# Kernel optimization log

Hardware: AMD Instinct MI355X
Metric: run time of the kernel (lower is better)

Reference implementation:

```python
import jax, jax.numpy as jnp
import numpy as np

NUM_HEADS = 4
SCALE = 0.1767766952966369  # head_dim**-0.5, head_dim=32


def setup_inputs() -> dict:
    key = jax.random.key(0)
    k1, k2, k3 = jax.random.split(key, 3)
    B, N, C = 4096, 49, 384  # B = 64 images * 64 windows, N = 7*7, C = 3*embed_dims
    qkv = jax.random.normal(k1, (B, N, C), dtype=jnp.float32)
    mask = jax.random.normal(k2, (NUM_HEADS, N, N), dtype=jnp.float32)
    rotate_mask = jax.random.normal(k3, (64, N, N), dtype=jnp.float32)  # nW = 64
    hw_pad = jnp.array([56, 56], dtype=jnp.int32)  # metadata only, unused in math
    return {"qkv": qkv, "mask": mask, "rotate_mask": rotate_mask, "hw_pad": hw_pad}


def reference(qkv, mask, rotate_mask, hw_pad):
    B, N, C = qkv.shape
    H = NUM_HEADS
    hd = C // H // 3
    # [B,N,3,H,hd] -> [3,B,H,N,hd]
    qkv_r = qkv.reshape(B, N, 3, H, hd).transpose(2, 0, 3, 1, 4)
    q, k, v = qkv_r[0] * SCALE, qkv_r[1], qkv_r[2]
    attn = jnp.einsum('bhqd,bhkd->bhqk', q, k) + mask  # mask broadcasts over B
    nW = rotate_mask.shape[0]
    # shifted-window mask: add per-window rotate mask, broadcast over image batch and heads
    attn = attn.reshape(B // nW, nW, H, N, N) + rotate_mask[None, :, None, :, :]
    attn = jax.nn.softmax(attn.reshape(B, H, N, N), axis=-1)
    out = jnp.einsum('bhqk,bhkd->bhqd', attn, v)  # [B,H,N,hd]
    return out.transpose(0, 2, 1, 3).reshape(B, N, C // 3)
```

## Files before the change

kernel.cpp:

```cpp
#include <hip/hip_runtime.h>

#define NTOK 49
#define NH 4
#define HD 32
#define CIN 384
#define NW 64
#define NPAD 64
#define QKP 136
#define SCALE_F 0.1767766952966369f

typedef _Float16 f16x8 __attribute__((ext_vector_type(8)));
typedef float f32x16 __attribute__((ext_vector_type(16)));
typedef __fp16 fp16x2 __attribute__((ext_vector_type(2)));

__device__ __forceinline__ unsigned int pkh(float a, float b) {
    fp16x2 h = __builtin_amdgcn_cvt_pkrtz(a, b);
    return __builtin_bit_cast(unsigned int, h);
}

__global__ __launch_bounds__(64) void prep_cmask(
    const float* __restrict__ mask,
    const float* __restrict__ rot,
    float* __restrict__ cmT)
{
    const int wh = blockIdx.x;
    const int w = wh >> 2, h = wh & 3;
    const int i = threadIdx.x;
    for (int j = 0; j < NPAD; ++j) {
        float v;
        if (j >= NTOK) v = -1e30f;
        else if (i >= NTOK) v = 0.f;
        else v = mask[(h * NTOK + i) * NTOK + j] + rot[(w * NTOK + i) * NTOK + j];
        cmT[((size_t)wh * NPAD + j) * NPAD + i] = v;
    }
}

template<bool USE_CM>
__global__ __launch_bounds__(512) void win_attn_mfma(
    const float* __restrict__ qkv,
    const float* __restrict__ mask,
    const float* __restrict__ rot,
    const float* __restrict__ cmT,
    float* __restrict__ out)
{
    const int b = blockIdx.x;
    const int w = b & (NW - 1);
    const int tid = threadIdx.x;
    const int wid = tid >> 6;
    const int h = wid >> 1;
    const int it = wid & 1;
    const int lane = tid & 63;
    const int l31 = lane & 31;
    const int hl = lane >> 5;

    __shared__ _Float16 Qs[NPAD * QKP];
    __shared__ _Float16 Ks[NPAD * QKP];

    const float* base = qkv + (size_t)b * (NTOK * CIN);

    for (int e = tid; e < NTOK * 64; e += 512) {
        const int n = e >> 6;
        const int c = e & 63;
        const int col = c * 4;
        const float4 f = *reinterpret_cast<const float4*>(base + n * CIN + col);
        uint2 u;
        if (col < 128) {
            u.x = pkh(f.x * SCALE_F, f.y * SCALE_F);
            u.y = pkh(f.z * SCALE_F, f.w * SCALE_F);
            *reinterpret_cast<uint2*>(&Qs[n * QKP + col]) = u;
        } else {
            u.x = pkh(f.x, f.y);
            u.y = pkh(f.z, f.w);
            *reinterpret_cast<uint2*>(&Ks[n * QKP + (col - 128)]) = u;
        }
    }
    for (int e = tid; e < 15 * 64; e += 512) {
        const int n = NTOK + (e >> 6);
        const int c = e & 63;
        const int col = c * 4;
        const uint2 z = make_uint2(0u, 0u);
        if (col < 128) *reinterpret_cast<uint2*>(&Qs[n * QKP + col]) = z;
        else           *reinterpret_cast<uint2*>(&Ks[n * QKP + (col - 128)]) = z;
    }

    const int i = l31 + 32 * it;
    float cm[2][16];
    #pragma unroll
    for (int jt = 0; jt < 2; ++jt) {
        #pragma unroll
        for (int r = 0; r < 16; ++r) {
            const int j = (r & 3) + 8 * (r >> 2) + 4 * hl + 32 * jt;
            if (USE_CM) {
                cm[jt][r] = cmT[((size_t)(w * 4 + h) * NPAD + j) * NPAD + i];
            } else {
                float v;
                if (j >= NTOK) v = -1e30f;
                else if (i >= NTOK) v = 0.f;
                else v = mask[(h * NTOK + i) * NTOK + j] + rot[(w * NTOK + i) * NTOK + j];
                cm[jt][r] = v;
            }
        }
    }

    __syncthreads();

    f16x8 ka[2][2], qa[2];
    #pragma unroll
    for (int kt = 0; kt < 2; ++kt) {
        #pragma unroll
        for (int ks = 0; ks < 2; ++ks) {
            ka[kt][ks] = *reinterpret_cast<const f16x8*>(&Ks[(l31 + 32 * kt) * QKP + h * HD + ks * 16 + hl * 8]);
        }
    }
    #pragma unroll
    for (int ks = 0; ks < 2; ++ks) {
        qa[ks] = *reinterpret_cast<const f16x8*>(&Qs[(l31 + 32 * it) * QKP + h * HD + ks * 16 + hl * 8]);
    }

    f32x16 acc[2];
    #pragma unroll
    for (int jt = 0; jt < 2; ++jt) {
        f32x16 a;
        #pragma unroll
        for (int r = 0; r < 16; ++r) a[r] = 0.f;
        a = __builtin_amdgcn_mfma_f32_32x32x16_f16(ka[jt][0], qa[0], a, 0, 0, 0);
        a = __builtin_amdgcn_mfma_f32_32x32x16_f16(ka[jt][1], qa[1], a, 0, 0, 0);
        acc[jt] = a;
    }

    float m = -3e38f;
    #pragma unroll
    for (int jt = 0; jt < 2; ++jt) {
        #pragma unroll
        for (int r = 0; r < 16; ++r) {
            acc[jt][r] += cm[jt][r];
            m = fmaxf(m, acc[jt][r]);
        }
    }
    m = fmaxf(m, __shfl_xor(m, 32));
    float s = 0.f;
    #pragma unroll
    for (int jt = 0; jt < 2; ++jt) {
        #pragma unroll
        for (int r = 0; r < 16; ++r) {
            const float e = __expf(acc[jt][r] - m);
            acc[jt][r] = e;
            s += e;
        }
    }
    s += __shfl_xor(s, 32);
    const float inv = 1.f / s;
    #pragma unroll
    for (int jt = 0; jt < 2; ++jt) {
        #pragma unroll
        for (int r = 0; r < 16; ++r) acc[jt][r] *= inv;
    }

    f32x16 oacc;
    #pragma unroll
    for (int r = 0; r < 16; ++r) oacc[r] = 0.f;

    #pragma unroll
    for (int ks = 0; ks < 4; ++ks) {
        unsigned int vd[4];
        #pragma unroll
        for (int ep = 0; ep < 4; ++ep) {
            const int j0 = 16 * ks + 8 * hl + 2 * ep;
            float v0 = 0.f, v1 = 0.f;
            if (j0 < NTOK)
                v0 = qkv[((size_t)b * NTOK + j0) * CIN + 256 + h * HD + l31];
            if (j0 + 1 < NTOK)
                v1 = qkv[((size_t)b * NTOK + j0 + 1) * CIN + 256 + h * HD + l31];
            vd[ep] = pkh(v0, v1);
        }
        uint4 vu = make_uint4(vd[0], vd[1], vd[2], vd[3]);
        const f16x8 vb = __builtin_bit_cast(f16x8, vu);

        const int jt = ks >> 1;
        const int r8 = 8 * (ks & 1);
        const unsigned lo0 = pkh(acc[jt][r8 + 0], acc[jt][r8 + 1]);
        const unsigned lo1 = pkh(acc[jt][r8 + 2], acc[jt][r8 + 3]);
        const unsigned hi0 = pkh(acc[jt][r8 + 4], acc[jt][r8 + 5]);
        const unsigned hi1 = pkh(acc[jt][r8 + 6], acc[jt][r8 + 7]);
        const unsigned x0 = hl ? lo0 : hi0;
        const unsigned x1 = hl ? lo1 : hi1;
        const unsigned y0 = (unsigned)__shfl_xor((int)x0, 32);
        const unsigned y1 = (unsigned)__shfl_xor((int)x1, 32);
        uint4 pu;
        pu.x = hl ? y0 : lo0;
        pu.y = hl ? y1 : lo1;
        pu.z = hl ? hi0 : y0;
        pu.w = hl ? hi1 : y1;
        const f16x8 pa = __builtin_bit_cast(f16x8, pu);
        oacc = __builtin_amdgcn_mfma_f32_32x32x16_f16(pa, vb, oacc, 0, 0, 0);
    }

    float* obase = out + (size_t)b * NTOK * (NH * HD) + h * HD + l31;
    #pragma unroll
    for (int r = 0; r < 16; ++r) {
        const int io = (r & 3) + 8 * (r >> 2) + 4 * hl + 32 * it;
        if (io < NTOK) obase[(size_t)io * (NH * HD)] = oacc[r];
    }
}

extern "C" void kernel_launch(void* const* d_in, const int* in_sizes, int n_in,
                              void* d_out, int out_size, void* d_ws, size_t ws_size,
                              hipStream_t stream) {
    const float* qkv  = (const float*)d_in[0];
    const float* mask = (const float*)d_in[1];
    const float* rot  = (const float*)d_in[2];
    float* out = (float*)d_out;

    const int Btot = in_sizes[0] / (NTOK * CIN);
    dim3 grid(Btot);

    const size_t cm_bytes = (size_t)NW * NH * NPAD * NPAD * sizeof(float);
    if (ws_size >= cm_bytes && d_ws != nullptr) {
        float* cmT = (float*)d_ws;
        prep_cmask<<<dim3(NW * NH), 64, 0, stream>>>(mask, rot, cmT);
        win_attn_mfma<true><<<grid, 512, 0, stream>>>(qkv, mask, rot, cmT, out);
    } else {
        win_attn_mfma<false><<<grid, 512, 0, stream>>>(qkv, mask, rot, nullptr, out);
    }
}
```

Baseline: 108.2 us.

## Stage V in shared memory with coalesced loads and fold mask into MFMA init

V is now loaded together with Q and K in one unrolled, coalesced float4 pass and converted to fp16 in shared memory. The old per-element strided global V reads inside the PV loop are removed. Zero-padding of rows 49-63 is merged into the same loop. The combined mask is used as the initial MFMA accumulator instead of being added afterward, which costs extra LDS and may lower occupancy.

```diff
diff --git a/kernel.cpp b/kernel.cpp
--- a/kernel.cpp
+++ b/kernel.cpp
@@ -6,7 +6,8 @@
 #define CIN 384
 #define NW 64
 #define NPAD 64
-#define QKP 136
+#define QS 136
+#define VS 132
 #define SCALE_F 0.1767766952966369f
 
 typedef _Float16 f16x8 __attribute__((ext_vector_type(8)));
@@ -53,34 +54,34 @@
     const int l31 = lane & 31;
     const int hl = lane >> 5;
 
-    __shared__ _Float16 Qs[NPAD * QKP];
-    __shared__ _Float16 Ks[NPAD * QKP];
+    __shared__ _Float16 Qs[NPAD * QS];
+    __shared__ _Float16 Ks[NPAD * QS];
+    __shared__ unsigned short Vs[NPAD * VS];
 
     const float* base = qkv + (size_t)b * (NTOK * CIN);
 
-    for (int e = tid; e < NTOK * 64; e += 512) {
-        const int n = e >> 6;
-        const int c = e & 63;
+    #pragma unroll
+    for (int t = 0; t < 12; ++t) {
+        const int e = tid + t * 512;
+        const int n = e / 96;
+        const int c = e % 96;
         const int col = c * 4;
-        const float4 f = *reinterpret_cast<const float4*>(base + n * CIN + col);
+        float4 f = make_float4(0.f, 0.f, 0.f, 0.f);
+        if (n < NTOK) f = *reinterpret_cast<const float4*>(base + n * CIN + col);
         uint2 u;
         if (col < 128) {
             u.x = pkh(f.x * SCALE_F, f.y * SCALE_F);
             u.y = pkh(f.z * SCALE_F, f.w * SCALE_F);
-            *reinterpret_cast<uint2*>(&Qs[n * QKP + col]) = u;
+            *reinterpret_cast<uint2*>(&Qs[n * QS + col]) = u;
+        } else if (col < 256) {
+            u.x = pkh(f.x, f.y);
+            u.y = pkh(f.z, f.w);
+            *reinterpret_cast<uint2*>(&Ks[n * QS + (col - 128)]) = u;
         } else {
             u.x = pkh(f.x, f.y);
             u.y = pkh(f.z, f.w);
-            *reinterpret_cast<uint2*>(&Ks[n * QKP + (col - 128)]) = u;
-        }
-    }
-    for (int e = tid; e < 15 * 64; e += 512) {
-        const int n = NTOK + (e >> 6);
-        const int c = e & 63;
-        const int col = c * 4;
-        const uint2 z = make_uint2(0u, 0u);
-        if (col < 128) *reinterpret_cast<uint2*>(&Qs[n * QKP + col]) = z;
-        else           *reinterpret_cast<uint2*>(&Ks[n * QKP + (col - 128)]) = z;
+            *reinterpret_cast<uint2*>(&Vs[n * VS + (col - 256)]) = u;
+        }
     }
 
     const int i = l31 + 32 * it;
@@ -109,12 +110,12 @@
     for (int kt = 0; kt < 2; ++kt) {
         #pragma unroll
         for (int ks = 0; ks < 2; ++ks) {
-            ka[kt][ks] = *reinterpret_cast<const f16x8*>(&Ks[(l31 + 32 * kt) * QKP + h * HD + ks * 16 + hl * 8]);
+            ka[kt][ks] = *reinterpret_cast<const f16x8*>(&Ks[(l31 + 32 * kt) * QS + h * HD + ks * 16 + hl * 8]);
         }
     }
     #pragma unroll
     for (int ks = 0; ks < 2; ++ks) {
-        qa[ks] = *reinterpret_cast<const f16x8*>(&Qs[(l31 + 32 * it) * QKP + h * HD + ks * 16 + hl * 8]);
+        qa[ks] = *reinterpret_cast<const f16x8*>(&Qs[(l31 + 32 * it) * QS + h * HD + ks * 16 + hl * 8]);
     }
 
     f32x16 acc[2];
@@ -122,7 +123,7 @@
     for (int jt = 0; jt < 2; ++jt) {
         f32x16 a;
         #pragma unroll
-        for (int r = 0; r < 16; ++r) a[r] = 0.f;
+        for (int r = 0; r < 16; ++r) a[r] = cm[jt][r];
         a = __builtin_amdgcn_mfma_f32_32x32x16_f16(ka[jt][0], qa[0], a, 0, 0, 0);
         a = __builtin_amdgcn_mfma_f32_32x32x16_f16(ka[jt][1], qa[1], a, 0, 0, 0);
         acc[jt] = a;
@@ -132,10 +133,7 @@
     #pragma unroll
     for (int jt = 0; jt < 2; ++jt) {
         #pragma unroll
-        for (int r = 0; r < 16; ++r) {
-            acc[jt][r] += cm[jt][r];
-            m = fmaxf(m, acc[jt][r]);
-        }
+        for (int r = 0; r < 16; ++r) m = fmaxf(m, acc[jt][r]);
     }
     m = fmaxf(m, __shfl_xor(m, 32));
     float s = 0.f;
@@ -164,14 +162,11 @@
     for (int ks = 0; ks < 4; ++ks) {
         unsigned int vd[4];
         #pragma unroll
-        for (int ep = 0; ep < 4; ++ep) {
-            const int j0 = 16 * ks + 8 * hl + 2 * ep;
-            float v0 = 0.f, v1 = 0.f;
-            if (j0 < NTOK)
-                v0 = qkv[((size_t)b * NTOK + j0) * CIN + 256 + h * HD + l31];
-            if (j0 + 1 < NTOK)
-                v1 = qkv[((size_t)b * NTOK + j0 + 1) * CIN + 256 + h * HD + l31];
-            vd[ep] = pkh(v0, v1);
+        for (int p = 0; p < 4; ++p) {
+            const int j0 = 16 * ks + 8 * hl + 2 * p;
+            const unsigned lo = Vs[j0 * VS + h * HD + l31];
+            const unsigned hi = Vs[(j0 + 1) * VS + h * HD + l31];
+            vd[p] = lo | (hi << 16);
         }
         uint4 vu = make_uint4(vd[0], vd[1], vd[2], vd[3]);
         const f16x8 vb = __builtin_bit_cast(f16x8, vu);
```

New measurement: 113.5 us. 1.05x slower.
